# Kernel tuning notes

Measured on AMD Instinct MI355X. Metric: run time of the kernel, lower is better.

The kernel has to match this reference:

```python
import jax, jax.numpy as jnp
import numpy as np

B, IN, H, L = 128, 256, 1024, 256
nA, nB = H // 2, (H - 1) // 2        # pairs per A-layer / B-layer
LB = L // 2
LA = L - LB                           # A layers come first when L is odd
PI = float(np.pi)


def setup_inputs() -> dict:
    key = jax.random.key(0)
    ks = jax.random.split(key, 14)
    u = lambda k, shp: jax.random.uniform(k, shp, minval=-PI, maxval=PI)
    return {
        "inputsR": jax.random.normal(ks[0], (B, IN), dtype=jnp.float32),
        "inputsI": jax.random.normal(ks[1], (B, IN), dtype=jnp.float32),
        "stateR": jax.random.normal(ks[2], (B, H), dtype=jnp.float32),
        "stateI": jax.random.normal(ks[3], (B, H), dtype=jnp.float32),
        # CLinear params (init_scale=0.01 inside RNNCellCmplx)
        "weightR": 0.01 * jax.random.normal(ks[4], (H, IN), dtype=jnp.float32),
        "weightI": 0.01 * jax.random.normal(ks[5], (H, IN), dtype=jnp.float32),
        "biasR": 0.01 * jax.random.normal(ks[6], (H,), dtype=jnp.float32),
        "biasI": 0.01 * jax.random.normal(ks[7], (H,), dtype=jnp.float32),
        # Clements mesh angles, uniform(-pi, pi)
        "angleA0": u(ks[8], (LA, nA)),
        "angleA1": u(ks[9], (LA, nA)),
        "angleB0": u(ks[10], (LB, nB)),
        "angleB1": u(ks[11], (LB, nB)),
        # diagonal phase + modReLU bias (both init to zero)
        "omega": jnp.zeros((H,), dtype=jnp.float32),
        "mod_bias": jnp.zeros((H,), dtype=jnp.float32),
    }


def _mzi(ar, ai, br, bi, th0, th1):
    """PSDC MZI on channel pairs: phase shifter e^{i*th0} on arm a, then a
    directional coupler with coupling angle th1 (unitary 2x2)."""
    c0, s0 = jnp.cos(th0), jnp.sin(th0)
    pr = c0 * ar - s0 * ai          # p = e^{i th0} * a
    pi_ = s0 * ar + c0 * ai
    c, s = jnp.cos(th1), jnp.sin(th1)
    oar = c * pr - s * bi           # a' = cos*p + i sin*b
    oai = c * pi_ + s * br
    obr = c * br - s * pi_          # b' = i sin*p + cos*b
    obi = c * bi + s * pr
    return oar, oai, obr, obi


def _layerA(xr, xi, t0, t1):
    Bs, N = xr.shape
    oar, oai, obr, obi = _mzi(xr[:, 0::2], xi[:, 0::2], xr[:, 1::2], xi[:, 1::2], t0, t1)
    xr = jnp.stack([oar, obr], axis=-1).reshape(Bs, N)
    xi = jnp.stack([oai, obi], axis=-1).reshape(Bs, N)
    return xr, xi


def _layerB(xr, xi, t0, t1):
    Bs, N = xr.shape  # pairs (1,2),(3,4),... ; channels 0 and N-1 pass through
    oar, oai, obr, obi = _mzi(xr[:, 1:-1:2], xi[:, 1:-1:2], xr[:, 2::2], xi[:, 2::2], t0, t1)
    midr = jnp.stack([oar, obr], axis=-1).reshape(Bs, N - 2)
    midi = jnp.stack([oai, obi], axis=-1).reshape(Bs, N - 2)
    xr = jnp.concatenate([xr[:, :1], midr, xr[:, -1:]], axis=1)
    xi = jnp.concatenate([xi[:, :1], midi, xi[:, -1:]], axis=1)
    return xr, xi


def _clements(xr, xi, A0, A1, B0, B1):
    def step(carry, ang):
        cr, ci = carry
        a0, a1, b0, b1 = ang
        cr, ci = _layerA(cr, ci, a0, a1)
        cr, ci = _layerB(cr, ci, b0, b1)
        return (cr, ci), None
    (xr, xi), _ = jax.lax.scan(step, (xr, xi), (A0[:LB], A1[:LB], B0, B1))
    for k in range(LB, LA):  # trailing A layer when num_layers is odd (static)
        xr, xi = _layerA(xr, xi, A0[k], A1[k])
    return xr, xi


def _forward(inputsR, inputsI, stateR, stateI, weightR, weightI, biasR, biasI,
             angleA0, angleA1, angleB0, angleB1, omega, mod_bias):
    # CLinear: complex y = W x + b
    ihR = inputsR @ weightR.T - inputsI @ weightI.T + biasR
    ihI = inputsR @ weightI.T + inputsI @ weightR.T + biasI
    # Clements unitary mesh on hidden state
    hr, hi = _clements(stateR, stateI, angleA0, angleA1, angleB0, angleB1)
    # diagonal phase e^{i omega}
    co, so = jnp.cos(omega), jnp.sin(omega)
    hhR = co * hr - so * hi
    hhI = so * hr + co * hi
    # complex add
    zr = ihR + hhR
    zi = ihI + hhI
    # modReLU: relu(|z| + b) * z / |z|
    mag = jnp.sqrt(zr * zr + zi * zi)
    scale = jax.nn.relu(mag + mod_bias) / jnp.maximum(mag, 1e-8)
    return jnp.stack([scale * zr, scale * zi])  # (2, B, H)


def reference(inputsR, inputsI, stateR, stateI, weightR, weightI, biasR, biasI,
              angleA0, angleA1, angleB0, angleB1, omega, mod_bias):
    return _forward(inputsR, inputsI, stateR, stateI, weightR, weightI, biasR, biasI,
                    angleA0, angleA1, angleB0, angleB1, omega, mod_bias)
```

## Files before the change

kernel.cpp:

```cpp
#include <hip/hip_runtime.h>
#include <math.h>

typedef float v2 __attribute__((ext_vector_type(2)));

#define NBATCH 128
#define NIN    256
#define NH     1024
#define NSTEPS 128
#define NB     511

#define TAB_F4_PER_L 1024
#define IH_OFF (NSTEPS * TAB_F4_PER_L * 4)

#define GEMM_BLOCKS 256
#define TRIG_BLOCKS 512

static __device__ __forceinline__ v2 to2(float a, float b) { v2 r; r.x = a; r.y = b; return r; }

__global__ __launch_bounds__(256) void prep_kernel(
    const float* __restrict__ inR, const float* __restrict__ inI,
    const float* __restrict__ wR,  const float* __restrict__ wI,
    const float* __restrict__ biasR, const float* __restrict__ biasI,
    const float* __restrict__ A0, const float* __restrict__ A1,
    const float* __restrict__ B0, const float* __restrict__ B1,
    float* __restrict__ ws)
{
    __shared__ v2 xs[256][17];
    __shared__ v2 wsh[32][34];

    if (blockIdx.x >= GEMM_BLOCKS) {
        int idx = (blockIdx.x - GEMM_BLOCKS) * 256 + threadIdx.x;
        int l = idx >> 10;
        int s = idx & 1023;
        int j = s >> 6, lane = s & 63;
        float a0, a1;
        bool ident = false;
        if (j < 8) {
            int p = 8 * lane + j;
            a0 = A0[l * 512 + p]; a1 = A1[l * 512 + p];
        } else {
            int p = 8 * lane + (j - 8);
            if (p < NB) { a0 = B0[l * NB + p]; a1 = B1[l * NB + p]; }
            else ident = true;
        }
        float4 v;
        if (ident) v = make_float4(1.f, 0.f, 1.f, 0.f);
        else {
            float s0, c0, s1, c1;
            __sincosf(a0, &s0, &c0);
            __sincosf(a1, &s1, &c1);
            v = make_float4(c0, s0, c1, s1);
        }
        ((float4*)ws)[l * TAB_F4_PER_L + j * 64 + lane] = v;
        return;
    }

    const int ht = blockIdx.x >> 3, bt = blockIdx.x & 7;
    const int h0 = ht * 32, b0 = bt * 16;
    const int tid = threadIdx.x;

    {
        int b = tid >> 4, k4 = tid & 15;
#pragma unroll
        for (int p = 0; p < 4; ++p) {
            int k0 = p * 64 + k4 * 4;
            float4 vr = *(const float4*)(inR + (b0 + b) * NIN + k0);
            float4 vi = *(const float4*)(inI + (b0 + b) * NIN + k0);
            xs[k0 + 0][b] = to2(vr.x, vi.x);
            xs[k0 + 1][b] = to2(vr.y, vi.y);
            xs[k0 + 2][b] = to2(vr.z, vi.z);
            xs[k0 + 3][b] = to2(vr.w, vi.w);
        }
    }

    const int hg = tid & 15, bl = tid >> 4;
    v2 acc0 = to2(0.f, 0.f), acc1 = to2(0.f, 0.f);

    for (int c = 0; c < 8; ++c) {
        __syncthreads();
        {
            int hh = tid >> 3, k4 = tid & 7;
            float4 vr = *(const float4*)(wR + (h0 + hh) * NIN + c * 32 + k4 * 4);
            float4 vi = *(const float4*)(wI + (h0 + hh) * NIN + c * 32 + k4 * 4);
            wsh[k4 * 4 + 0][hh] = to2(vr.x, vi.x);
            wsh[k4 * 4 + 1][hh] = to2(vr.y, vi.y);
            wsh[k4 * 4 + 2][hh] = to2(vr.z, vi.z);
            wsh[k4 * 4 + 3][hh] = to2(vr.w, vi.w);
        }
        __syncthreads();
#pragma unroll
        for (int k = 0; k < 32; ++k) {
            float4 wv = *(const float4*)&wsh[k][hg * 2];
            v2 w0 = to2(wv.x, wv.y), w1 = to2(wv.z, wv.w);
            v2 xv = xs[c * 32 + k][bl];
            acc0 += to2(xv.x, xv.x) * w0 + to2(xv.y, xv.y) * to2(-w0.y, w0.x);
            acc1 += to2(xv.x, xv.x) * w1 + to2(xv.y, xv.y) * to2(-w1.y, w1.x);
        }
    }
    int h = h0 + hg * 2, b = b0 + bl;
    acc0 += to2(biasR[h], biasI[h]);
    acc1 += to2(biasR[h + 1], biasI[h + 1]);
    ((float4*)(ws + IH_OFF))[b * 512 + (h >> 1)] =
        make_float4(acc0.x, acc0.y, acc1.x, acc1.y);
}

__device__ __forceinline__ void mzi(const float4 t, v2& a, v2& b)
{
    v2 P  = to2(t.x, t.y) * to2(a.x, a.x) + to2(-t.y, t.x) * to2(a.y, a.y);
    v2 na = to2(t.z, t.z) * P + to2(-t.w, t.w) * to2(b.y, b.x);
    b     = to2(t.z, t.z) * b + to2(-t.w, t.w) * to2(P.y, P.x);
    a = na;
}

__device__ __forceinline__ void step(v2* x, const float4* T, int lane)
{
    mzi(T[0], x[0], x[1]);
    mzi(T[7], x[14], x[15]);
    float rc0r  = __shfl_down(x[0].x, 1, 64);
    float rc0i  = __shfl_down(x[0].y, 1, 64);
    float lc15r = __shfl_up(x[15].x, 1, 64);
    float lc15i = __shfl_up(x[15].y, 1, 64);
    float blx = __shfl_up(T[15].x, 1, 64);
    float bly = __shfl_up(T[15].y, 1, 64);
    float blz = __shfl_up(T[15].z, 1, 64);
    float blw = __shfl_up(T[15].w, 1, 64);
    if (lane == 0) { blx = 1.f; bly = 0.f; blz = 1.f; blw = 0.f; }
#pragma unroll
    for (int j = 1; j < 7; ++j) mzi(T[j], x[2 * j], x[2 * j + 1]);
#pragma unroll
    for (int j = 0; j < 7; ++j) mzi(T[8 + j], x[2 * j + 1], x[2 * j + 2]);
    {
        const float4 t = T[15];
        v2 P = to2(t.x, t.y) * to2(x[15].x, x[15].x) + to2(-t.y, t.x) * to2(x[15].y, x[15].y);
        x[15] = to2(t.z, t.z) * P + to2(-t.w, t.w) * to2(rc0i, rc0r);
    }
    {
        v2 P = to2(blx, bly) * to2(lc15r, lc15r) + to2(-bly, blx) * to2(lc15i, lc15i);
        x[0] = to2(blz, blz) * x[0] + to2(-blw, blw) * to2(P.y, P.x);
    }
}

#define LOADL(T, l)                                                       \
    do {                                                                  \
        const float4* _p = tab + (l) * TAB_F4_PER_L + lane;               \
        _Pragma("unroll") for (int _j = 0; _j < 16; ++_j)                 \
            T[_j] = _p[_j * 64];                                          \
    } while (0)

__global__ __launch_bounds__(64, 1) void mesh_kernel(
    const float* __restrict__ stateR, const float* __restrict__ stateI,
    const float* __restrict__ omega,  const float* __restrict__ mod_bias,
    const float* __restrict__ ws, float* __restrict__ out)
{
    const int b = blockIdx.x;
    const int lane = threadIdx.x;
    const float4* tab = (const float4*)ws;

    v2 x[16];
    {
        const float4* sr4 = (const float4*)(stateR + b * NH + lane * 16);
        const float4* si4 = (const float4*)(stateI + b * NH + lane * 16);
#pragma unroll
        for (int q = 0; q < 4; ++q) {
            float4 r = sr4[q], i = si4[q];
            x[4 * q + 0] = to2(r.x, i.x);
            x[4 * q + 1] = to2(r.y, i.y);
            x[4 * q + 2] = to2(r.z, i.z);
            x[4 * q + 3] = to2(r.w, i.w);
        }
    }

    float4 Ta[16], Tb[16];
    LOADL(Ta, 0);
    for (int l = 0; l < NSTEPS; l += 2) {
        LOADL(Tb, l + 1);
        __builtin_amdgcn_sched_barrier(0);
        step(x, Ta, lane);
        {
            int ln = (l + 2 < NSTEPS) ? l + 2 : NSTEPS - 1;
            LOADL(Ta, ln);
        }
        __builtin_amdgcn_sched_barrier(0);
        step(x, Tb, lane);
    }

    float om[16], mb[16];
#pragma unroll
    for (int q = 0; q < 4; ++q) {
        float4 o = ((const float4*)(omega + lane * 16))[q];
        float4 m = ((const float4*)(mod_bias + lane * 16))[q];
        om[4 * q] = o.x; om[4 * q + 1] = o.y; om[4 * q + 2] = o.z; om[4 * q + 3] = o.w;
        mb[4 * q] = m.x; mb[4 * q + 1] = m.y; mb[4 * q + 2] = m.z; mb[4 * q + 3] = m.w;
    }
    float o0[16], o1[16];
    const float4* ihp = (const float4*)(ws + IH_OFF + b * NH * 2) + lane * 8;
#pragma unroll
    for (int q = 0; q < 8; ++q) {
        float4 ih2 = ihp[q];
#pragma unroll
        for (int e = 0; e < 2; ++e) {
            int j = 2 * q + e;
            float ihr = (e == 0) ? ih2.x : ih2.z;
            float ihi = (e == 0) ? ih2.y : ih2.w;
            float so, co;
            __sincosf(om[j], &so, &co);
            float zr = ihr + co * x[j].x - so * x[j].y;
            float zi = ihi + so * x[j].x + co * x[j].y;
            float mag = sqrtf(zr * zr + zi * zi);
            float sc = fmaxf(mag + mb[j], 0.f) / fmaxf(mag, 1e-8f);
            o0[j] = sc * zr;
            o1[j] = sc * zi;
        }
    }
#pragma unroll
    for (int q = 0; q < 4; ++q) {
        ((float4*)(out + b * NH + lane * 16))[q] =
            make_float4(o0[4 * q], o0[4 * q + 1], o0[4 * q + 2], o0[4 * q + 3]);
        ((float4*)(out + NBATCH * NH + b * NH + lane * 16))[q] =
            make_float4(o1[4 * q], o1[4 * q + 1], o1[4 * q + 2], o1[4 * q + 3]);
    }
}

extern "C" void kernel_launch(void* const* d_in, const int* in_sizes, int n_in,
                              void* d_out, int out_size, void* d_ws, size_t ws_size,
                              hipStream_t stream)
{
    const float* inputsR = (const float*)d_in[0];
    const float* inputsI = (const float*)d_in[1];
    const float* stateR  = (const float*)d_in[2];
    const float* stateI  = (const float*)d_in[3];
    const float* weightR = (const float*)d_in[4];
    const float* weightI = (const float*)d_in[5];
    const float* biasR   = (const float*)d_in[6];
    const float* biasI   = (const float*)d_in[7];
    const float* angleA0 = (const float*)d_in[8];
    const float* angleA1 = (const float*)d_in[9];
    const float* angleB0 = (const float*)d_in[10];
    const float* angleB1 = (const float*)d_in[11];
    const float* omega   = (const float*)d_in[12];
    const float* mod_b   = (const float*)d_in[13];
    float* ws = (float*)d_ws;
    float* out = (float*)d_out;

    hipLaunchKernelGGL(prep_kernel, dim3(GEMM_BLOCKS + TRIG_BLOCKS), dim3(256),
                       0, stream, inputsR, inputsI, weightR, weightI,
                       biasR, biasI, angleA0, angleA1, angleB0, angleB1, ws);
    hipLaunchKernelGGL(mesh_kernel, dim3(NBATCH), dim3(64), 0, stream,
                       stateR, stateI, omega, mod_b, ws, out);
}
```

Measured before the change: 158.6 us.

## Split mesh rows across four wavefronts with LDS boundary exchange per layer

The mesh kernel moves from one 64-thread wavefront per batch row, with 16 channels per lane, to a 256-thread block with 4 channels per thread. The trig table layout changes to match. Neighbour values across wavefront boundaries now go through shared memory, guarded by a __syncthreads each step. This cuts the serial per-lane arithmetic per layer by about four times and raises the thread count, at the cost of 128 block-wide barriers and more scattered table loads per thread.

After: 151.3 us. -4.6%, faster.

```diff
diff --git a/kernel.cpp b/kernel.cpp
--- a/kernel.cpp
+++ b/kernel.cpp
@@ -32,14 +32,14 @@
         int idx = (blockIdx.x - GEMM_BLOCKS) * 256 + threadIdx.x;
         int l = idx >> 10;
         int s = idx & 1023;
-        int j = s >> 6, lane = s & 63;
+        int j = s >> 8, g = s & 255;
         float a0, a1;
         bool ident = false;
-        if (j < 8) {
-            int p = 8 * lane + j;
+        if (j < 2) {
+            int p = 2 * g + j;
             a0 = A0[l * 512 + p]; a1 = A1[l * 512 + p];
         } else {
-            int p = 8 * lane + (j - 8);
+            int p = 2 * g + (j - 2);
             if (p < NB) { a0 = B0[l * NB + p]; a1 = B1[l * NB + p]; }
             else ident = true;
         }
@@ -51,7 +51,7 @@
             __sincosf(a1, &s1, &c1);
             v = make_float4(c0, s0, c1, s1);
         }
-        ((float4*)ws)[l * TAB_F4_PER_L + j * 64 + lane] = v;
+        ((float4*)ws)[l * TAB_F4_PER_L + j * 256 + g] = v;
         return;
     }
 
@@ -112,113 +112,103 @@
     a = na;
 }
 
-__device__ __forceinline__ void step(v2* x, const float4* T, int lane)
+__device__ __forceinline__ void stepf(v2 x[4], const float4* T, const float4 TL,
+                                      int w, int lane, int par,
+                                      v2 (&sA0)[2][4], v2 (&sA3)[2][4])
 {
     mzi(T[0], x[0], x[1]);
-    mzi(T[7], x[14], x[15]);
-    float rc0r  = __shfl_down(x[0].x, 1, 64);
-    float rc0i  = __shfl_down(x[0].y, 1, 64);
-    float lc15r = __shfl_up(x[15].x, 1, 64);
-    float lc15i = __shfl_up(x[15].y, 1, 64);
-    float blx = __shfl_up(T[15].x, 1, 64);
-    float bly = __shfl_up(T[15].y, 1, 64);
-    float blz = __shfl_up(T[15].z, 1, 64);
-    float blw = __shfl_up(T[15].w, 1, 64);
-    if (lane == 0) { blx = 1.f; bly = 0.f; blz = 1.f; blw = 0.f; }
-#pragma unroll
-    for (int j = 1; j < 7; ++j) mzi(T[j], x[2 * j], x[2 * j + 1]);
-#pragma unroll
-    for (int j = 0; j < 7; ++j) mzi(T[8 + j], x[2 * j + 1], x[2 * j + 2]);
-    {
-        const float4 t = T[15];
-        v2 P = to2(t.x, t.y) * to2(x[15].x, x[15].x) + to2(-t.y, t.x) * to2(x[15].y, x[15].y);
-        x[15] = to2(t.z, t.z) * P + to2(-t.w, t.w) * to2(rc0i, rc0r);
-    }
-    {
-        v2 P = to2(blx, bly) * to2(lc15r, lc15r) + to2(-bly, blx) * to2(lc15i, lc15i);
-        x[0] = to2(blz, blz) * x[0] + to2(-blw, blw) * to2(P.y, P.x);
-    }
-}
-
-#define LOADL(T, l)                                                       \
+    mzi(T[1], x[2], x[3]);
+    float rcr = __shfl_down(x[0].x, 1, 64);
+    float rci = __shfl_down(x[0].y, 1, 64);
+    float lcr = __shfl_up(x[3].x, 1, 64);
+    float lci = __shfl_up(x[3].y, 1, 64);
+    if (lane == 0)  sA0[par][w] = x[0];
+    if (lane == 63) sA3[par][w] = x[3];
+    __syncthreads();
+    if (lane == 63 && w < 3) { v2 t = sA0[par][w + 1]; rcr = t.x; rci = t.y; }
+    if (lane == 0  && w > 0) { v2 t = sA3[par][w - 1]; lcr = t.x; lci = t.y; }
+    mzi(T[2], x[1], x[2]);
+    {
+        const float4 t = T[3];
+        v2 P = to2(t.x, t.y) * to2(x[3].x, x[3].x) + to2(-t.y, t.x) * to2(x[3].y, x[3].y);
+        x[3] = to2(t.z, t.z) * P + to2(-t.w, t.w) * to2(rci, rcr);
+    }
+    {
+        v2 P = to2(TL.x, TL.y) * to2(lcr, lcr) + to2(-TL.y, TL.x) * to2(lci, lci);
+        x[0] = to2(TL.z, TL.z) * x[0] + to2(-TL.w, TL.w) * to2(P.y, P.x);
+    }
+}
+
+#define LOADL(T, TL, l)                                                   \
     do {                                                                  \
-        const float4* _p = tab + (l) * TAB_F4_PER_L + lane;               \
-        _Pragma("unroll") for (int _j = 0; _j < 16; ++_j)                 \
-            T[_j] = _p[_j * 64];                                          \
+        const float4* _p = tab + (l) * TAB_F4_PER_L + g;                  \
+        T[0] = _p[0];                                                     \
+        T[1] = _p[256];                                                   \
+        T[2] = _p[512];                                                   \
+        T[3] = _p[768];                                                   \
+        TL = _p[767];                                     \
+        if (g == 0) TL = make_float4(1.f, 0.f, 1.f, 0.f);                 \
     } while (0)
 
-__global__ __launch_bounds__(64, 1) void mesh_kernel(
+__global__ __launch_bounds__(256, 1) void mesh_kernel(
     const float* __restrict__ stateR, const float* __restrict__ stateI,
     const float* __restrict__ omega,  const float* __restrict__ mod_bias,
     const float* __restrict__ ws, float* __restrict__ out)
 {
     const int b = blockIdx.x;
-    const int lane = threadIdx.x;
+    const int g = threadIdx.x;
+    const int lane = g & 63;
+    const int w = g >> 6;
     const float4* tab = (const float4*)ws;
 
-    v2 x[16];
-    {
-        const float4* sr4 = (const float4*)(stateR + b * NH + lane * 16);
-        const float4* si4 = (const float4*)(stateI + b * NH + lane * 16);
-#pragma unroll
-        for (int q = 0; q < 4; ++q) {
-            float4 r = sr4[q], i = si4[q];
-            x[4 * q + 0] = to2(r.x, i.x);
-            x[4 * q + 1] = to2(r.y, i.y);
-            x[4 * q + 2] = to2(r.z, i.z);
-            x[4 * q + 3] = to2(r.w, i.w);
-        }
-    }
-
-    float4 Ta[16], Tb[16];
-    LOADL(Ta, 0);
+    __shared__ v2 sA0[2][4];
+    __shared__ v2 sA3[2][4];
+
+    v2 x[4];
+    {
+        float4 r = *(const float4*)(stateR + b * NH + 4 * g);
+        float4 i = *(const float4*)(stateI + b * NH + 4 * g);
+        x[0] = to2(r.x, i.x);
+        x[1] = to2(r.y, i.y);
+        x[2] = to2(r.z, i.z);
+        x[3] = to2(r.w, i.w);
+    }
+
+    float4 Ta[4], Tb[4], TLa, TLb;
+    LOADL(Ta, TLa, 0);
     for (int l = 0; l < NSTEPS; l += 2) {
-        LOADL(Tb, l + 1);
-        __builtin_amdgcn_sched_barrier(0);
-        step(x, Ta, lane);
+        LOADL(Tb, TLb, l + 1);
+        stepf(x, Ta, TLa, w, lane, 0, sA0, sA3);
         {
             int ln = (l + 2 < NSTEPS) ? l + 2 : NSTEPS - 1;
-            LOADL(Ta, ln);
-        }
-        __builtin_amdgcn_sched_barrier(0);
-        step(x, Tb, lane);
-    }
-
-    float om[16], mb[16];
+            LOADL(Ta, TLa, ln);
+        }
+        stepf(x, Tb, TLb, w, lane, 1, sA0, sA3);
+    }
+
+    float4 o4 = *(const float4*)(omega + 4 * g);
+    float4 m4 = *(const float4*)(mod_bias + 4 * g);
+    const float4* ihp = (const float4*)(ws + IH_OFF) + b * 512 + 2 * g;
+    float4 ih0 = ihp[0], ih1 = ihp[1];
+
+    float om[4] = { o4.x, o4.y, o4.z, o4.w };
+    float mb[4] = { m4.x, m4.y, m4.z, m4.w };
+    float ihr[4] = { ih0.x, ih0.z, ih1.x, ih1.z };
+    float ihi[4] = { ih0.y, ih0.w, ih1.y, ih1.w };
+    float oR[4], oI[4];
 #pragma unroll
-    for (int q = 0; q < 4; ++q) {
-        float4 o = ((const float4*)(omega + lane * 16))[q];
-        float4 m = ((const float4*)(mod_bias + lane * 16))[q];
-        om[4 * q] = o.x; om[4 * q + 1] = o.y; om[4 * q + 2] = o.z; om[4 * q + 3] = o.w;
-        mb[4 * q] = m.x; mb[4 * q + 1] = m.y; mb[4 * q + 2] = m.z; mb[4 * q + 3] = m.w;
-    }
-    float o0[16], o1[16];
-    const float4* ihp = (const float4*)(ws + IH_OFF + b * NH * 2) + lane * 8;
-#pragma unroll
-    for (int q = 0; q < 8; ++q) {
-        float4 ih2 = ihp[q];
-#pragma unroll
-        for (int e = 0; e < 2; ++e) {
-            int j = 2 * q + e;
-            float ihr = (e == 0) ? ih2.x : ih2.z;
-            float ihi = (e == 0) ? ih2.y : ih2.w;
-            float so, co;
-            __sincosf(om[j], &so, &co);
-            float zr = ihr + co * x[j].x - so * x[j].y;
-            float zi = ihi + so * x[j].x + co * x[j].y;
-            float mag = sqrtf(zr * zr + zi * zi);
-            float sc = fmaxf(mag + mb[j], 0.f) / fmaxf(mag, 1e-8f);
-            o0[j] = sc * zr;
-            o1[j] = sc * zi;
-        }
-    }
-#pragma unroll
-    for (int q = 0; q < 4; ++q) {
-        ((float4*)(out + b * NH + lane * 16))[q] =
-            make_float4(o0[4 * q], o0[4 * q + 1], o0[4 * q + 2], o0[4 * q + 3]);
-        ((float4*)(out + NBATCH * NH + b * NH + lane * 16))[q] =
-            make_float4(o1[4 * q], o1[4 * q + 1], o1[4 * q + 2], o1[4 * q + 3]);
-    }
+    for (int j = 0; j < 4; ++j) {
+        float so, co;
+        __sincosf(om[j], &so, &co);
+        float zr = ihr[j] + co * x[j].x - so * x[j].y;
+        float zi = ihi[j] + so * x[j].x + co * x[j].y;
+        float mag = sqrtf(zr * zr + zi * zi);
+        float sc = fmaxf(mag + mb[j], 0.f) / fmaxf(mag, 1e-8f);
+        oR[j] = sc * zr;
+        oI[j] = sc * zi;
+    }
+    *(float4*)(out + b * NH + 4 * g) = make_float4(oR[0], oR[1], oR[2], oR[3]);
+    *(float4*)(out + NBATCH * NH + b * NH + 4 * g) = make_float4(oI[0], oI[1], oI[2], oI[3]);
 }
 
 extern "C" void kernel_launch(void* const* d_in, const int* in_sizes, int n_in,
@@ -245,6 +235,6 @@
     hipLaunchKernelGGL(prep_kernel, dim3(GEMM_BLOCKS + TRIG_BLOCKS), dim3(256),
                        0, stream, inputsR, inputsI, weightR, weightI,
                        biasR, biasI, angleA0, angleA1, angleB0, angleB1, ws);
-    hipLaunchKernelGGL(mesh_kernel, dim3(NBATCH), dim3(64), 0, stream,
+    hipLaunchKernelGGL(mesh_kernel, dim3(NBATCH), dim3(256), 0, stream,
                        stateR, stateI, omega, mod_b, ws, out);
 }
```
